# Optimization experiments

Measured on AMD Instinct MI355X. Metric: run time of the kernel, lower is better.

Reference implementation:

```python
import jax, jax.numpy as jnp
import numpy as np

E = 1024   # embd_size
H = 16     # head_count
HS = E // H
B = 8
T = 1024   # seq len == input_size
EPS = 1e-5

def _ln(x, g, b):
    m = jnp.mean(x, axis=-1, keepdims=True)
    v = jnp.mean((x - m) ** 2, axis=-1, keepdims=True)
    return (x - m) * jax.lax.rsqrt(v + EPS) * g + b

def setup_inputs() -> dict:
    key = jax.random.key(0)
    ks = jax.random.split(key, 12)
    s_attn = 1.0 / np.sqrt(E)
    s_ff1 = 1.0 / np.sqrt(E)
    s_ff2 = 1.0 / np.sqrt(4 * E)
    return {
        "x": jax.random.normal(ks[0], (B, T, E), dtype=jnp.float32),
        "wq": jax.random.normal(ks[1], (H, E, HS), dtype=jnp.float32) * s_attn,
        "wk": jax.random.normal(ks[2], (H, E, HS), dtype=jnp.float32) * s_attn,
        "wv": jax.random.normal(ks[3], (H, E, HS), dtype=jnp.float32) * s_attn,
        "w_proj": jax.random.normal(ks[4], (E, E), dtype=jnp.float32) * s_attn,
        "b_proj": jnp.zeros((E,), dtype=jnp.float32),
        "w1": jax.random.normal(ks[5], (E, 4 * E), dtype=jnp.float32) * s_ff1,
        "b1": jnp.zeros((4 * E,), dtype=jnp.float32),
        "w2": jax.random.normal(ks[6], (4 * E, E), dtype=jnp.float32) * s_ff2,
        "b2": jnp.zeros((E,), dtype=jnp.float32),
        "g1": jnp.ones((E,), dtype=jnp.float32),
        "be1": jnp.zeros((E,), dtype=jnp.float32),
        "g2": jnp.ones((E,), dtype=jnp.float32),
        "be2": jnp.zeros((E,), dtype=jnp.float32),
    }

def reference(x, wq, wk, wv, w_proj, b_proj, w1, b1, w2, b2, g1, be1, g2, be2):
    Tn = x.shape[1]
    h = _ln(x, g1, be1)
    # per-head projections, batched over heads: [B,T,E] x [H,E,S] -> [B,H,T,S]
    q = jnp.einsum('bte,hes->bhts', h, wq)
    k = jnp.einsum('bte,hes->bhts', h, wk)
    v = jnp.einsum('bte,hes->bhts', h, wv)
    scores = jnp.einsum('bhts,bhus->bhtu', q, k)
    # NOTE: source multiplies by sqrt(T) (x.shape[2] of scores), not 1/sqrt(head_size)
    scores = scores * jnp.float32(Tn) ** 0.5
    causal = jnp.tril(jnp.ones((Tn, Tn), dtype=bool))
    scores = jnp.where(causal, scores, -jnp.inf)
    attn = jax.nn.softmax(scores, axis=-1)
    out = jnp.einsum('bhtu,bhus->bhts', attn, v)           # [B,H,T,S]
    out = out.transpose(0, 2, 1, 3).reshape(x.shape[0], Tn, E)  # concat heads
    out = out @ w_proj + b_proj
    x = x + out
    f = _ln(x, g2, be2)
    f = jax.nn.relu(f @ w1 + b1) @ w2 + b2
    return x + f
```

## Files before the change

### kernel.cpp

```cpp
#include <hip/hip_runtime.h>


typedef unsigned short u16;
typedef __attribute__((ext_vector_type(8))) short  bfx8;
typedef __attribute__((ext_vector_type(4))) float  f32x4;
typedef __attribute__((ext_vector_type(4))) unsigned short u16v4;

#define MFMA16 __builtin_amdgcn_mfma_f32_16x16x32_bf16

__device__ __forceinline__ u16 f2bf(float f) {
    union { float f; unsigned u; } c; c.f = f;
    unsigned r = c.u + 0x7fffu + ((c.u >> 16) & 1u);
    return (u16)(r >> 16);
}
__device__ __forceinline__ float bf2f(u16 b) {
    union { unsigned u; float f; } c; c.u = ((unsigned)b) << 16; return c.f;
}
__device__ __forceinline__ float exp2_fast(float x) {
    float r; asm("v_exp_f32 %0, %1" : "=v"(r) : "v"(x)); return r;
}

__device__ __forceinline__ void gl_lds16(const void* g, void* l) {
    void* gg = (void*)g;
    __builtin_amdgcn_global_load_lds(
        (__attribute__((address_space(1))) void*)gg,
        (__attribute__((address_space(3))) void*)l,
        16, 0, 0);
}

__device__ __forceinline__ void transpose_tile(const float* __restrict__ src,
                                               u16* __restrict__ dhi,
                                               u16* __restrict__ dlo,
                                               int C, int OS, int row0, int col0)
{
    __shared__ float t[64][65];
    const int tid = threadIdx.x;
    const float* s = src + ((size_t)row0) * C + col0;
    const size_t obase = ((size_t)col0) * OS + row0;
    {
        const int r = tid >> 2, c4 = (tid & 3) * 16;
#pragma unroll
        for (int k = 0; k < 4; ++k) {
            float4 f = *(const float4*)(s + (size_t)r * C + c4 + k * 4);
            t[r][c4 + k*4 + 0] = f.x; t[r][c4 + k*4 + 1] = f.y;
            t[r][c4 + k*4 + 2] = f.z; t[r][c4 + k*4 + 3] = f.w;
        }
    }
    __syncthreads();
    {
        const int c = tid >> 2, r4 = (tid & 3) * 16;
        bfx8 h0, h1, l0, l1;
#pragma unroll
        for (int k = 0; k < 8; ++k) {
            float v0 = t[r4 + k][c];
            float v1 = t[r4 + 8 + k][c];
            u16 a = f2bf(v0), b = f2bf(v1);
            h0[k] = (short)a; h1[k] = (short)b;
            l0[k] = (short)f2bf(v0 - bf2f(a));
            l1[k] = (short)f2bf(v1 - bf2f(b));
        }
        u16* d = dhi + obase + (size_t)c * OS + r4;
        *(bfx8*)d = h0; *(bfx8*)(d + 8) = h1;
        if (dlo) {
            u16* d2 = dlo + obase + (size_t)c * OS + r4;
            *(bfx8*)d2 = l0; *(bfx8*)(d2 + 8) = l1;
        }
    }
}

__global__ __launch_bounds__(256)
void repack_qkv(const float* __restrict__ wq, const float* __restrict__ wk,
                const float* __restrict__ wv, u16* __restrict__ qkhi,
                u16* __restrict__ qklo, u16* __restrict__ vT)
{
    const int sel = blockIdx.x;
    const int yt  = blockIdx.y;
    const int hh  = blockIdx.z;
    const float* src = (sel == 0) ? wq : (sel == 1) ? wk : wv;
    u16* dhi = (sel == 0) ? qkhi : (sel == 1) ? (qkhi + (size_t)1024 * 1024) : vT;
    u16* dlo = (sel == 0) ? qklo : (sel == 1) ? (qklo + (size_t)1024 * 1024) : nullptr;
    transpose_tile(src + (size_t)hh * 65536,
                   dhi + (size_t)hh * 65536,
                   dlo ? dlo + (size_t)hh * 65536 : nullptr,
                   64, 1024, yt * 64, 0);
}

__global__ __launch_bounds__(256)
void repack_w(const float* __restrict__ wp, u16* __restrict__ wpT,
              const float* __restrict__ w1, u16* __restrict__ w1T,
              const float* __restrict__ w2, u16* __restrict__ w2T)
{
    const int id = blockIdx.x;
    if (id < 256) {
        const int xt = id & 15, yt = id >> 4;
        transpose_tile(wp, wpT, nullptr, 1024, 1024, yt * 64, xt * 64);
    } else if (id < 1280) {
        const int i2 = id - 256;
        const int xt = i2 & 63, yt = i2 >> 6;
        transpose_tile(w1, w1T, nullptr, 4096, 1024, yt * 64, xt * 64);
    } else {
        const int i2 = id - 1280;
        const int xt = i2 & 15, yt = i2 >> 4;
        transpose_tile(w2, w2T, nullptr, 1024, 4096, yt * 64, xt * 64);
    }
}

__global__ __launch_bounds__(256)
void ln_split(const float* __restrict__ x, const float* __restrict__ g,
              const float* __restrict__ be, u16* __restrict__ hhi,
              u16* __restrict__ hlo)
{
    const int row = blockIdx.x;
    const int tid = threadIdx.x;
    const float4 v = ((const float4*)(x + (size_t)row * 1024))[tid];
    float s  = v.x + v.y + v.z + v.w;
    float s2 = v.x*v.x + v.y*v.y + v.z*v.z + v.w*v.w;
#pragma unroll
    for (int m = 32; m >= 1; m >>= 1) {
        s  += __shfl_xor(s,  m, 64);
        s2 += __shfl_xor(s2, m, 64);
    }
    __shared__ float rs[4], rq[4];
    if ((tid & 63) == 0) { rs[tid >> 6] = s; rq[tid >> 6] = s2; }
    __syncthreads();
    s  = rs[0] + rs[1] + rs[2] + rs[3];
    s2 = rq[0] + rq[1] + rq[2] + rq[3];
    const float mean = s * (1.0f / 1024.0f);
    const float var  = s2 * (1.0f / 1024.0f) - mean * mean;
    const float inv  = rsqrtf(var + 1e-5f);
    const int col0 = tid * 4;
    float hv[4];
    hv[0] = (v.x - mean) * inv * g[col0+0] + be[col0+0];
    hv[1] = (v.y - mean) * inv * g[col0+1] + be[col0+1];
    hv[2] = (v.z - mean) * inv * g[col0+2] + be[col0+2];
    hv[3] = (v.w - mean) * inv * g[col0+3] + be[col0+3];
    u16v4 hb, lb;
#pragma unroll
    for (int k = 0; k < 4; ++k) {
        u16 a = f2bf(hv[k]);
        hb[k] = a;
        lb[k] = f2bf(hv[k] - bf2f(a));
    }
    *(u16v4*)(hhi + (size_t)row * 1024 + col0) = hb;
    if (hlo) *(u16v4*)(hlo + (size_t)row * 1024 + col0) = lb;
}

#define BM 128
#define BN 128
#define BKT 32

template<int FLAGS>
__global__ __launch_bounds__(256, 2)
void gemm_bt(const u16* __restrict__ A, const u16* __restrict__ Bt,
             void* __restrict__ Cout, const float* __restrict__ bias,
             const float* __restrict__ res, int M, int N, int K)
{
    __shared__ u16 As[BM * BKT];
    __shared__ u16 Bs[BN * BKT];
    const int tid  = threadIdx.x;
    const int lane = tid & 63, wave = tid >> 6;
    const int wr = wave >> 1, wc = wave & 1;
    const int li = lane & 15, lg = lane >> 4;

    const int nbx = gridDim.x;
    const int nwg = nbx * gridDim.y;
    const int cpx = nwg >> 3;
    int bid = blockIdx.y * nbx + blockIdx.x;
    bid = (bid & 7) * cpx + (bid >> 3);
    const size_t m0 = (size_t)(bid / nbx) * BM;
    const size_t n0 = (size_t)(bid % nbx) * BN;
    f32x4 acc[4][4] = {};

    const int slot0 = tid, slot1 = tid + 256;
    const int r0 = slot0 >> 2, kc0 = (slot0 & 3) * 8;
    const int r1 = slot1 >> 2, kc1 = (slot1 & 3) * 8;

    for (int kt = 0; kt < K; kt += BKT) {
        __syncthreads();
        gl_lds16(A  + (m0 + r0) * K + kt + kc0, As + slot0 * 8);
        gl_lds16(Bt + (n0 + r0) * K + kt + kc0, Bs + slot0 * 8);
        gl_lds16(A  + (m0 + r1) * K + kt + kc1, As + slot1 * 8);
        gl_lds16(Bt + (n0 + r1) * K + kt + kc1, Bs + slot1 * 8);
        __syncthreads();
        bfx8 af[4], bfr[4];
#pragma unroll
        for (int i = 0; i < 4; ++i)
            af[i] = *(const bfx8*)&As[(wr * 64 + i * 16 + li) * BKT + lg * 8];
#pragma unroll
        for (int j = 0; j < 4; ++j)
            bfr[j] = *(const bfx8*)&Bs[(wc * 64 + j * 16 + li) * BKT + lg * 8];
#pragma unroll
        for (int i = 0; i < 4; ++i)
#pragma unroll
            for (int j = 0; j < 4; ++j)
                acc[i][j] = MFMA16(af[i], bfr[j], acc[i][j], 0, 0, 0);
    }

    float* Cf = (float*)Cout;
    u16*   Cb = (u16*)Cout;
#pragma unroll
    for (int i = 0; i < 4; ++i)
#pragma unroll
        for (int j = 0; j < 4; ++j)
#pragma unroll
            for (int r = 0; r < 4; ++r) {
                const size_t row = m0 + wr * 64 + i * 16 + lg * 4 + r;
                const size_t col = n0 + wc * 64 + j * 16 + li;
                float v = acc[i][j][r];
                if (FLAGS & 1) v += bias[col];
                if (FLAGS & 2) v = fmaxf(v, 0.0f);
                if (FLAGS & 4) v += res[row * (size_t)N + col];
                if (FLAGS & 16) {
                    const size_t drow = ((col >> 10) * 16 + (row >> 6)) * 64 + (row & 63);
                    Cb[drow * 1024 + (col & 1023)] = f2bf(v);
                } else if (FLAGS & 8) {
                    Cf[row * (size_t)N + col] = v;
                } else {
                    Cb[row * (size_t)N + col] = f2bf(v);
                }
            }
}

template<int EPI, int SPLIT3>
__global__ __launch_bounds__(512, 2)
void gemm8(const u16* __restrict__ A, const u16* __restrict__ Al,
           const u16* __restrict__ Bt, const u16* __restrict__ Bl,
           u16* __restrict__ C, u16* __restrict__ Clo,
           const float* __restrict__ bias,
           int M, int N, int K, int NBX)
{
    __shared__ u16 Asl[2][2][128 * 64];
    __shared__ u16 Bsl[2][2][128 * 64];
    const int tid = threadIdx.x;
    const int lane = tid & 63, wave = tid >> 6;
    const int wr = wave >> 2, wc = wave & 3;
    const int li = lane & 15, lg = lane >> 4;

    const int bid = blockIdx.x;
    const int nwg = gridDim.x;
    const int cpx = nwg >> 3;
    const int swz = (bid & 7) * cpx + (bid >> 3);
    const int bx = swz % NBX, by = swz / NBX;
    const size_t m0 = (size_t)by * 256, n0 = (size_t)bx * 256;

    char* ldsA = (char*)&Asl[0][0][0];
    char* ldsB = (char*)&Bsl[0][0][0];

    const int KT = K >> 6;

    auto stageA = [&](int j, int h) {
        const u16* src = A;
        int jj = j;
        if (SPLIT3) {
            src = (j < 2 * KT) ? A : Al;
            jj = (j < KT) ? j : ((j < 2 * KT) ? j - KT : j - 2 * KT);
        }
#pragma unroll
        for (int site = 0; site < 2; ++site) {
            const int s = tid + site * 512;
            const int r = s >> 3;
            const int cb = ((s & 7) << 4) ^ ((r & 7) << 4);
            gl_lds16((const char*)(src + (m0 + h * 128 + r) * (size_t)K + (size_t)jj * 64) + cb,
                     ldsA + ((j & 1) * 2 + h) * 16384 + s * 16);
        }
    };
    auto stageB = [&](int j, int h) {
        const u16* src = Bt;
        int jj = j;
        if (SPLIT3) {
            src = (j < KT) ? Bt : ((j < 2 * KT) ? Bl : Bt);
            jj = (j < KT) ? j : ((j < 2 * KT) ? j - KT : j - 2 * KT);
        }
#pragma unroll
        for (int site = 0; site < 2; ++site) {
            const int s = tid + site * 512;
            const int r = s >> 3;
            const int cb = ((s & 7) << 4) ^ ((r & 7) << 4);
            gl_lds16((const char*)(src + (n0 + h * 128 + r) * (size_t)K + (size_t)jj * 64) + cb,
                     ldsB + ((j & 1) * 2 + h) * 16384 + s * 16);
        }
    };

    const int lsw = (li & 7) << 4;
    const int aHalfBase = wr * 16384;
    const int bHalfBase = (wc >> 1) * 16384;
    const int bRow0 = (wc & 1) * 64;

    f32x4 acc[8][4] = {};
    const int NT = SPLIT3 ? 3 * KT : KT;
    const int NI = NT >> 1;

    stageA(0, 0); stageA(0, 1); stageB(0, 0); stageB(0, 1);
    stageB(1, 0); stageB(1, 1);
    asm volatile("s_waitcnt vmcnt(0)" ::: "memory");
    __builtin_amdgcn_sched_barrier(0);
    __builtin_amdgcn_s_barrier();
    __builtin_amdgcn_sched_barrier(0);

    for (int t = 0; t < NI; ++t) {
        const bool more = (t + 1 < NI);
#pragma unroll
        for (int half = 0; half < 2; ++half) {
            const int buf = half;
            const int abase = buf * 32768 + aHalfBase;
            const int bbase = buf * 32768 + bHalfBase;
            bfx8 bfr[4][2];
#pragma unroll
            for (int q = 0; q < 4; ++q) {
                if (q == 0) {
#pragma unroll
                    for (int nf = 0; nf < 4; ++nf)
#pragma unroll
                        for (int ks = 0; ks < 2; ++ks)
                            bfr[nf][ks] = *(const bfx8*)(ldsB + bbase
                                + (bRow0 + nf * 16 + li) * 128
                                + ((ks * 64 + lg * 16) ^ lsw));
                }
                bfx8 afr[2][2];
#pragma unroll
                for (int m = 0; m < 2; ++m)
#pragma unroll
                    for (int ks = 0; ks < 2; ++ks)
                        afr[m][ks] = *(const bfx8*)(ldsA + abase
                            + ((2 * q + m) * 16 + li) * 128
                            + ((ks * 64 + lg * 16) ^ lsw));

                if (half == 0) {
                    if (q == 0) stageA(2 * t + 1, 0);
                    else if (q == 1) stageA(2 * t + 1, 1);
                    else if (q == 2) { if (more) stageB(2 * t + 2, 0); }
                    else             { if (more) stageB(2 * t + 2, 1); }
                } else {
                    if (q == 0)      { if (more) stageA(2 * t + 2, 0); }
                    else if (q == 1) { if (more) stageA(2 * t + 2, 1); }
                    else if (q == 2) { if (more) stageB(2 * t + 3, 0); }
                    else             { if (more) stageB(2 * t + 3, 1); }
                }

                __builtin_amdgcn_sched_barrier(0);
                __builtin_amdgcn_s_barrier();
                asm volatile("s_waitcnt lgkmcnt(0)" ::: "memory");
                __builtin_amdgcn_sched_barrier(0);
                __builtin_amdgcn_s_setprio(1);
#pragma unroll
                for (int ks = 0; ks < 2; ++ks)
#pragma unroll
                    for (int m = 0; m < 2; ++m)
#pragma unroll
                        for (int nf = 0; nf < 4; ++nf)
                            acc[2 * q + m][nf] = MFMA16(afr[m][ks], bfr[nf][ks],
                                                        acc[2 * q + m][nf], 0, 0, 0);
                __builtin_amdgcn_s_setprio(0);
                __builtin_amdgcn_sched_barrier(0);
                if (q == 3) {
                    if (half == 0) {
                        if (more) { asm volatile("s_waitcnt vmcnt(4)" ::: "memory"); }
                        else      { asm volatile("s_waitcnt vmcnt(0)" ::: "memory"); }
                    } else if (more) {
                        asm volatile("s_waitcnt vmcnt(4)" ::: "memory");
                    }
                    __builtin_amdgcn_sched_barrier(0);
                }
                __builtin_amdgcn_s_barrier();
                __builtin_amdgcn_sched_barrier(0);
            }
        }
    }

#pragma unroll
    for (int i = 0; i < 8; ++i)
#pragma unroll
        for (int nf = 0; nf < 4; ++nf)
#pragma unroll
            for (int r = 0; r < 4; ++r) {
                const size_t row = m0 + wr * 128 + i * 16 + lg * 4 + r;
                const size_t col = n0 + wc * 64 + nf * 16 + li;
                if (EPI == 0) {
                    float v = acc[i][nf][r] + bias[col];
                    v = fmaxf(v, 0.0f);
                    C[row * (size_t)N + col] = f2bf(v);
                } else {
                    const float v = acc[i][nf][r];
                    const u16 hi = f2bf(v);
                    C[row * (size_t)N + col]   = hi;
                    Clo[row * (size_t)N + col] = f2bf(v - bf2f(hi));
                }
            }
}

#define QKS 2048

__global__ __launch_bounds__(256, 3)
void attn(const u16* __restrict__ qkhi, const u16* __restrict__ qklo,
          const u16* __restrict__ vt, u16* __restrict__ ao)
{
    const int id  = blockIdx.x;
    const int swz = (id & 7) * 256 + (id >> 3);
    const int qt  = 15 - (swz & 15);
    const int h   = (swz >> 4) & 15;
    const int b   = swz >> 8;

    const int tid = threadIdx.x;
    const int wave = tid >> 6, lane = tid & 63;
    const int li = lane & 15, lg = lane >> 4;

    __shared__ u16 KsHi[2][4096];
    __shared__ u16 KsLo[2][4096];
    __shared__ u16 Pl[64 * 64];

    const size_t qrow = (size_t)b * 1024 + qt * 64 + wave * 16 + li;
    const size_t qoff = qrow * QKS + h * 64 + lg * 8;
    const bfx8 qh0 = *(const bfx8*)(qkhi + qoff);
    const bfx8 qh1 = *(const bfx8*)(qkhi + qoff + 32);
    const bfx8 ql0 = *(const bfx8*)(qklo + qoff);
    const bfx8 ql1 = *(const bfx8*)(qklo + qoff + 32);

    bfx8 onesf;
#pragma unroll
    for (int k = 0; k < 8; ++k) onesf[k] = (short)0x3F80;

    f32x4 O[4] = {};
    f32x4 O5 = {0.f, 0.f, 0.f, 0.f};
    float mrow[4] = {-3e38f, -3e38f, -3e38f, -3e38f};

    const u16* kh_base = qkhi + ((size_t)b * 1024) * QKS + 1024 + h * 64;
    const u16* kl_base = qklo + ((size_t)b * 1024) * QKS + 1024 + h * 64;
    const u16* v_base  = vt + ((size_t)(b * 16 + h) * 64) * 1024;

    auto stageK = [&](int kt, int bufIdx) {
#pragma unroll
        for (int site = 0; site < 2; ++site) {
            const int s = tid + site * 256;
            const int r = s >> 3;
            const int cb = (((s & 7) << 4) ^ ((r & 7) << 4));
            const size_t go = ((size_t)(kt * 64 + r)) * QKS;
            gl_lds16((const char*)(kh_base + go) + cb, (char*)&KsHi[bufIdx][0] + s * 16);
            gl_lds16((const char*)(kl_base + go) + cb, (char*)&KsLo[bufIdx][0] + s * 16);
        }
    };

    const int rswz = (li & 7) << 4;
    char* pband = (char*)&Pl[0] + wave * 2048;

    stageK(0, 0);

    for (int kt = 0; kt <= qt; ++kt) {
        const int cur = kt & 1;

        bfx8 vld[2][4];
#pragma unroll
        for (int nf = 0; nf < 4; ++nf) {
            const u16* vr = v_base + ((size_t)(nf * 16 + li)) * 1024 + kt * 64 + lg * 8;
            vld[0][nf] = *(const bfx8*)vr;
            vld[1][nf] = *(const bfx8*)(vr + 32);
        }

        if (kt < qt) {
            stageK(kt + 1, cur ^ 1);
            asm volatile("s_waitcnt vmcnt(12)" ::: "memory");
        } else {
            asm volatile("s_waitcnt vmcnt(8)" ::: "memory");
        }
        __builtin_amdgcn_sched_barrier(0);
        __builtin_amdgcn_s_barrier();
        __builtin_amdgcn_sched_barrier(0);

        float sv[4][4];
        const char* khc = (const char*)&KsHi[cur][0];
        const char* klc = (const char*)&KsLo[cur][0];
#pragma unroll
        for (int nf = 0; nf < 4; ++nf) {
            const int rb = (nf * 16 + li) * 128;
            bfx8 kh0v = *(const bfx8*)(khc + rb + (((lg * 16) + 0 ) ^ rswz));
            bfx8 kh1v = *(const bfx8*)(khc + rb + (((lg * 16) + 64) ^ rswz));
            bfx8 kl0v = *(const bfx8*)(klc + rb + (((lg * 16) + 0 ) ^ rswz));
            bfx8 kl1v = *(const bfx8*)(klc + rb + (((lg * 16) + 64) ^ rswz));
            f32x4 a = {0.f, 0.f, 0.f, 0.f};
            a = MFMA16(qh0, kh0v, a, 0, 0, 0);
            a = MFMA16(qh1, kh1v, a, 0, 0, 0);
            a = MFMA16(qh0, kl0v, a, 0, 0, 0);
            a = MFMA16(qh1, kl1v, a, 0, 0, 0);
            a = MFMA16(ql0, kh0v, a, 0, 0, 0);
            a = MFMA16(ql1, kh1v, a, 0, 0, 0);
#pragma unroll
            for (int r = 0; r < 4; ++r) sv[nf][r] = a[r];
        }

        asm volatile("s_waitcnt lgkmcnt(0)" ::: "memory");
        __builtin_amdgcn_sched_barrier(0);
        __builtin_amdgcn_s_barrier();
        __builtin_amdgcn_sched_barrier(0);

        const float SC = 46.16624130844683f;
        float pmax[4] = {-3e38f, -3e38f, -3e38f, -3e38f};
        if (kt == qt) {
            const int rowg = qt * 64 + wave * 16 + lg * 4;
            const int colg = kt * 64 + li;
#pragma unroll
            for (int nf = 0; nf < 4; ++nf)
#pragma unroll
                for (int r = 0; r < 4; ++r) {
                    float x2 = sv[nf][r] * SC;
                    if (colg + nf * 16 > rowg + r) x2 = -3e38f;
                    sv[nf][r] = x2;
                    pmax[r] = fmaxf(pmax[r], x2);
                }
        } else {
#pragma unroll
            for (int nf = 0; nf < 4; ++nf)
#pragma unroll
                for (int r = 0; r < 4; ++r) {
                    const float x2 = sv[nf][r] * SC;
                    sv[nf][r] = x2;
                    pmax[r] = fmaxf(pmax[r], x2);
                }
        }
#pragma unroll
        for (int msk = 1; msk < 16; msk <<= 1)
#pragma unroll
            for (int r = 0; r < 4; ++r)
                pmax[r] = fmaxf(pmax[r], __shfl_xor(pmax[r], msk, 64));

        const bool grow = !__all((pmax[0] - mrow[0] <= 11.5416f) &&
                                 (pmax[1] - mrow[1] <= 11.5416f) &&
                                 (pmax[2] - mrow[2] <= 11.5416f) &&
                                 (pmax[3] - mrow[3] <= 11.5416f));
        if (grow) {
            float alr[4];
#pragma unroll
            for (int r = 0; r < 4; ++r) {
                const float mnew = fmaxf(mrow[r], pmax[r]);
                alr[r] = exp2_fast(mrow[r] - mnew);
                mrow[r] = mnew;
            }
#pragma unroll
            for (int nf = 0; nf < 4; ++nf)
#pragma unroll
                for (int r = 0; r < 4; ++r)
                    O[nf][r] *= alr[r];
#pragma unroll
            for (int r = 0; r < 4; ++r)
                O5[r] *= alr[r];
        }

#pragma unroll
        for (int nf = 0; nf < 4; ++nf)
#pragma unroll
            for (int r = 0; r < 4; ++r) {
                const int prow = lg * 4 + r;
                const int pb = prow * 128 + ((((nf * 16 + li) * 2)) ^ ((prow & 7) << 4));
                *(u16*)(pband + pb) = f2bf(exp2_fast(sv[nf][r] - mrow[r]));
            }

#pragma unroll
        for (int ku = 0; ku < 2; ++ku) {
            bfx8 pf = *(const bfx8*)(pband + li * 128
                                     + ((ku * 64 + lg * 16) ^ ((li & 7) << 4)));
#pragma unroll
            for (int nf = 0; nf < 4; ++nf)
                O[nf] = MFMA16(pf, vld[ku][nf], O[nf], 0, 0, 0);
            O5 = MFMA16(pf, onesf, O5, 0, 0, 0);
        }
    }

    float invl[4];
#pragma unroll
    for (int r = 0; r < 4; ++r) invl[r] = 1.0f / O5[r];
    const size_t orow = (size_t)b * 1024 + qt * 64 + wave * 16 + lg * 4;
#pragma unroll
    for (int nf = 0; nf < 4; ++nf)
#pragma unroll
        for (int r = 0; r < 4; ++r)
            ao[(orow + r) * 1024 + h * 64 + nf * 16 + li] = f2bf(O[nf][r] * invl[r]);
}

extern "C" void kernel_launch(void* const* d_in, const int* in_sizes, int n_in,
                              void* d_out, int out_size, void* d_ws, size_t ws_size,
                              hipStream_t stream)
{
    (void)in_sizes; (void)n_in; (void)out_size; (void)ws_size;
    const float* x      = (const float*)d_in[0];
    const float* wq     = (const float*)d_in[1];
    const float* wk     = (const float*)d_in[2];
    const float* wv     = (const float*)d_in[3];
    const float* w_proj = (const float*)d_in[4];
    const float* b_proj = (const float*)d_in[5];
    const float* w1     = (const float*)d_in[6];
    const float* b1     = (const float*)d_in[7];
    const float* w2     = (const float*)d_in[8];
    const float* b2     = (const float*)d_in[9];
    const float* g1     = (const float*)d_in[10];
    const float* be1    = (const float*)d_in[11];
    const float* g2     = (const float*)d_in[12];
    const float* be2    = (const float*)d_in[13];
    float* out = (float*)d_out;

    const size_t MB = (size_t)1024 * 1024;
    char* wsp = (char*)d_ws;
    u16* h_hi  = (u16*)(wsp + 0 * MB);
    u16* h_lo  = (u16*)(wsp + 16 * MB);
    u16* qk_hi = (u16*)(wsp + 32 * MB);
    u16* qk_lo = (u16*)(wsp + 64 * MB);
    u16* vtr   = (u16*)(wsp + 112 * MB);
    float* y   = (float*)(wsp + 128 * MB);
    u16* wqkT_hi = (u16*)(wsp + 160 * MB);
    u16* wqkT_lo = (u16*)(wsp + 164 * MB);
    u16* wvT     = (u16*)(wsp + 168 * MB);
    u16* wpT     = (u16*)(wsp + 170 * MB);
    u16* w1T     = (u16*)(wsp + 172 * MB);
    u16* w2T     = (u16*)(wsp + 180 * MB);
    u16* f2  = h_hi;
    u16* ao  = h_lo;
    u16* act = qk_hi;

    dim3 blk(256);

    repack_qkv<<<dim3(3, 16, 16), blk, 0, stream>>>(wq, wk, wv, wqkT_hi, wqkT_lo, wvT);
    repack_w<<<dim3(2304), blk, 0, stream>>>(w_proj, wpT, w1, w1T, w2, w2T);

    ln_split<<<8192, blk, 0, stream>>>(x, g1, be1, h_hi, h_lo);

    gemm8<1, 1><<<dim3(256), dim3(512), 0, stream>>>(h_hi, h_lo, wqkT_hi, wqkT_lo,
                                                     qk_hi, qk_lo, nullptr,
                                                     8192, 2048, 1024, 8);
    gemm_bt<16><<<dim3(64, 8), blk, 0, stream>>>(wvT, h_hi, vtr, nullptr, nullptr, 1024, 8192, 1024);

    attn<<<dim3(2048), blk, 0, stream>>>(qk_hi, qk_lo, vtr, ao);

    gemm_bt<1 | 4 | 8><<<dim3(8, 64), blk, 0, stream>>>(ao, wpT, y, b_proj, x, 8192, 1024, 1024);

    ln_split<<<8192, blk, 0, stream>>>(y, g2, be2, f2, nullptr);

    gemm8<0, 0><<<dim3(512), dim3(512), 0, stream>>>(f2, nullptr, w1T, nullptr,
                                                     act, nullptr, b1,
                                                     8192, 4096, 1024, 16);
    gemm_bt<1 | 4 | 8><<<dim3(8, 64), blk, 0, stream>>>(act, w2T, out, b2, y, 8192, 1024, 4096);
}
```

Baseline: 489.2 us.

## Stage K in 128-row pairs and halve barriers in causal attention loop

The attention kernel now stages two 64-key tiles per iteration into double-buffered LDS (now twice as large). It overlaps the second tile's QK MFMAs with the first tile's softmax and PV work, so the loop needs half as many block barriers. The intent is to cut synchronisation and load-latency stalls per key tile. The cost is more LDS per block (about 72KB), which may lower occupancy below the 3-blocks launch bound, plus more registers held for the second V tile.

```diff
diff --git a/kernel.cpp b/kernel.cpp
--- a/kernel.cpp
+++ b/kernel.cpp
@@ -404,8 +404,8 @@
     const int wave = tid >> 6, lane = tid & 63;
     const int li = lane & 15, lg = lane >> 4;
 
-    __shared__ u16 KsHi[2][4096];
-    __shared__ u16 KsLo[2][4096];
+    __shared__ u16 KsHi[2][8192];
+    __shared__ u16 KsLo[2][8192];
     __shared__ u16 Pl[64 * 64];
 
     const size_t qrow = (size_t)b * 1024 + qt * 64 + wave * 16 + li;
@@ -427,13 +427,13 @@
     const u16* kl_base = qklo + ((size_t)b * 1024) * QKS + 1024 + h * 64;
     const u16* v_base  = vt + ((size_t)(b * 16 + h) * 64) * 1024;
 
-    auto stageK = [&](int kt, int bufIdx) {
-#pragma unroll
-        for (int site = 0; site < 2; ++site) {
+    auto stagePair = [&](int p, int bufIdx) {
+#pragma unroll
+        for (int site = 0; site < 4; ++site) {
             const int s = tid + site * 256;
             const int r = s >> 3;
             const int cb = (((s & 7) << 4) ^ ((r & 7) << 4));
-            const size_t go = ((size_t)(kt * 64 + r)) * QKS;
+            const size_t go = ((size_t)(p * 128 + r)) * QKS;
             gl_lds16((const char*)(kh_base + go) + cb, (char*)&KsHi[bufIdx][0] + s * 16);
             gl_lds16((const char*)(kl_base + go) + cb, (char*)&KsLo[bufIdx][0] + s * 16);
         }
@@ -442,22 +442,100 @@
     const int rswz = (li & 7) << 4;
     char* pband = (char*)&Pl[0] + wave * 2048;
 
-    stageK(0, 0);
-
-    for (int kt = 0; kt <= qt; ++kt) {
-        const int cur = kt & 1;
-
-        bfx8 vld[2][4];
+    const float SC = 46.16624130844683f;
+
+    auto processTile = [&](float (&sv)[4][4], int kt, bfx8 (&vldX)[2][4]) {
+        float pmax[4] = {-3e38f, -3e38f, -3e38f, -3e38f};
+        if (kt == qt) {
+            const int rowg = qt * 64 + wave * 16 + lg * 4;
+            const int colg = kt * 64 + li;
+#pragma unroll
+            for (int nf = 0; nf < 4; ++nf)
+#pragma unroll
+                for (int r = 0; r < 4; ++r) {
+                    float x2 = sv[nf][r] * SC;
+                    if (colg + nf * 16 > rowg + r) x2 = -3e38f;
+                    sv[nf][r] = x2;
+                    pmax[r] = fmaxf(pmax[r], x2);
+                }
+        } else {
+#pragma unroll
+            for (int nf = 0; nf < 4; ++nf)
+#pragma unroll
+                for (int r = 0; r < 4; ++r) {
+                    const float x2 = sv[nf][r] * SC;
+                    sv[nf][r] = x2;
+                    pmax[r] = fmaxf(pmax[r], x2);
+                }
+        }
+#pragma unroll
+        for (int msk = 1; msk < 16; msk <<= 1)
+#pragma unroll
+            for (int r = 0; r < 4; ++r)
+                pmax[r] = fmaxf(pmax[r], __shfl_xor(pmax[r], msk, 64));
+
+        const bool grow = !__all((pmax[0] - mrow[0] <= 11.5416f) &&
+                                 (pmax[1] - mrow[1] <= 11.5416f) &&
+                                 (pmax[2] - mrow[2] <= 11.5416f) &&
+                                 (pmax[3] - mrow[3] <= 11.5416f));
+        if (grow) {
+            float alr[4];
+#pragma unroll
+            for (int r = 0; r < 4; ++r) {
+                const float mnew = fmaxf(mrow[r], pmax[r]);
+                alr[r] = exp2_fast(mrow[r] - mnew);
+                mrow[r] = mnew;
+            }
+#pragma unroll
+            for (int nf = 0; nf < 4; ++nf)
+#pragma unroll
+                for (int r = 0; r < 4; ++r)
+                    O[nf][r] *= alr[r];
+#pragma unroll
+            for (int r = 0; r < 4; ++r)
+                O5[r] *= alr[r];
+        }
+
+#pragma unroll
+        for (int nf = 0; nf < 4; ++nf)
+#pragma unroll
+            for (int r = 0; r < 4; ++r) {
+                const int prow = lg * 4 + r;
+                const int pb = prow * 128 + ((((nf * 16 + li) * 2)) ^ ((prow & 7) << 4));
+                *(u16*)(pband + pb) = f2bf(exp2_fast(sv[nf][r] - mrow[r]));
+            }
+
+#pragma unroll
+        for (int ku = 0; ku < 2; ++ku) {
+            bfx8 pf = *(const bfx8*)(pband + li * 128
+                                     + ((ku * 64 + lg * 16) ^ ((li & 7) << 4)));
+#pragma unroll
+            for (int nf = 0; nf < 4; ++nf)
+                O[nf] = MFMA16(pf, vldX[ku][nf], O[nf], 0, 0, 0);
+            O5 = MFMA16(pf, onesf, O5, 0, 0, 0);
+        }
+    };
+
+    const int nkt = qt + 1;
+    const int np  = (nkt + 1) >> 1;
+    stagePair(0, 0);
+
+    for (int p = 0; p < np; ++p) {
+        const int cur = p & 1;
+        const int kt0 = 2 * p;
+        const bool has1 = (kt0 + 1 < nkt);
+
+        bfx8 vld0[2][4];
 #pragma unroll
         for (int nf = 0; nf < 4; ++nf) {
-            const u16* vr = v_base + ((size_t)(nf * 16 + li)) * 1024 + kt * 64 + lg * 8;
-            vld[0][nf] = *(const bfx8*)vr;
-            vld[1][nf] = *(const bfx8*)(vr + 32);
-        }
-
-        if (kt < qt) {
-            stageK(kt + 1, cur ^ 1);
-            asm volatile("s_waitcnt vmcnt(12)" ::: "memory");
+            const u16* vr = v_base + ((size_t)(nf * 16 + li)) * 1024 + kt0 * 64 + lg * 8;
+            vld0[0][nf] = *(const bfx8*)vr;
+            vld0[1][nf] = *(const bfx8*)(vr + 32);
+        }
+
+        if (p + 1 < np) {
+            stagePair(p + 1, cur ^ 1);
+            asm volatile("s_waitcnt vmcnt(16)" ::: "memory");
         } else {
             asm volatile("s_waitcnt vmcnt(8)" ::: "memory");
         }
@@ -465,9 +543,10 @@
         __builtin_amdgcn_s_barrier();
         __builtin_amdgcn_sched_barrier(0);
 
-        float sv[4][4];
         const char* khc = (const char*)&KsHi[cur][0];
         const char* klc = (const char*)&KsLo[cur][0];
+
+        float sv[4][4];
 #pragma unroll
         for (int nf = 0; nf < 4; ++nf) {
             const int rb = (nf * 16 + li) * 128;
@@ -486,81 +565,45 @@
             for (int r = 0; r < 4; ++r) sv[nf][r] = a[r];
         }
 
+        bfx8 vld1[2][4];
+        if (has1) {
+#pragma unroll
+            for (int nf = 0; nf < 4; ++nf) {
+                const u16* vr = v_base + ((size_t)(nf * 16 + li)) * 1024 + (kt0 + 1) * 64 + lg * 8;
+                vld1[0][nf] = *(const bfx8*)vr;
+                vld1[1][nf] = *(const bfx8*)(vr + 32);
+            }
+        }
+
+        processTile(sv, kt0, vld0);
+
+        if (has1) {
+#pragma unroll
+            for (int nf = 0; nf < 4; ++nf) {
+                const int rb = (64 + nf * 16 + li) * 128;
+                bfx8 kh0v = *(const bfx8*)(khc + rb + (((lg * 16) + 0 ) ^ rswz));
+                bfx8 kh1v = *(const bfx8*)(khc + rb + (((lg * 16) + 64) ^ rswz));
+                bfx8 kl0v = *(const bfx8*)(klc + rb + (((lg * 16) + 0 ) ^ rswz));
+                bfx8 kl1v = *(const bfx8*)(klc + rb + (((lg * 16) + 64) ^ rswz));
+                f32x4 a = {0.f, 0.f, 0.f, 0.f};
+                a = MFMA16(qh0, kh0v, a, 0, 0, 0);
+                a = MFMA16(qh1, kh1v, a, 0, 0, 0);
+                a = MFMA16(qh0, kl0v, a, 0, 0, 0);
+                a = MFMA16(qh1, kl1v, a, 0, 0, 0);
+                a = MFMA16(ql0, kh0v, a, 0, 0, 0);
+                a = MFMA16(ql1, kh1v, a, 0, 0, 0);
+#pragma unroll
+                for (int r = 0; r < 4; ++r) sv[nf][r] = a[r];
+            }
+        }
+
         asm volatile("s_waitcnt lgkmcnt(0)" ::: "memory");
         __builtin_amdgcn_sched_barrier(0);
         __builtin_amdgcn_s_barrier();
         __builtin_amdgcn_sched_barrier(0);
 
-        const float SC = 46.16624130844683f;
-        float pmax[4] = {-3e38f, -3e38f, -3e38f, -3e38f};
-        if (kt == qt) {
-            const int rowg = qt * 64 + wave * 16 + lg * 4;
-            const int colg = kt * 64 + li;
-#pragma unroll
-            for (int nf = 0; nf < 4; ++nf)
-#pragma unroll
-                for (int r = 0; r < 4; ++r) {
-                    float x2 = sv[nf][r] * SC;
-                    if (colg + nf * 16 > rowg + r) x2 = -3e38f;
-                    sv[nf][r] = x2;
-                    pmax[r] = fmaxf(pmax[r], x2);
-                }
-        } else {
-#pragma unroll
-            for (int nf = 0; nf < 4; ++nf)
-#pragma unroll
-                for (int r = 0; r < 4; ++r) {
-                    const float x2 = sv[nf][r] * SC;
-                    sv[nf][r] = x2;
-                    pmax[r] = fmaxf(pmax[r], x2);
-                }
-        }
-#pragma unroll
-        for (int msk = 1; msk < 16; msk <<= 1)
-#pragma unroll
-            for (int r = 0; r < 4; ++r)
-                pmax[r] = fmaxf(pmax[r], __shfl_xor(pmax[r], msk, 64));
-
-        const bool grow = !__all((pmax[0] - mrow[0] <= 11.5416f) &&
-                                 (pmax[1] - mrow[1] <= 11.5416f) &&
-                                 (pmax[2] - mrow[2] <= 11.5416f) &&
-                                 (pmax[3] - mrow[3] <= 11.5416f));
-        if (grow) {
-            float alr[4];
-#pragma unroll
-            for (int r = 0; r < 4; ++r) {
-                const float mnew = fmaxf(mrow[r], pmax[r]);
-                alr[r] = exp2_fast(mrow[r] - mnew);
-                mrow[r] = mnew;
-            }
-#pragma unroll
-            for (int nf = 0; nf < 4; ++nf)
-#pragma unroll
-                for (int r = 0; r < 4; ++r)
-                    O[nf][r] *= alr[r];
-#pragma unroll
-            for (int r = 0; r < 4; ++r)
-                O5[r] *= alr[r];
-        }
-
-#pragma unroll
-        for (int nf = 0; nf < 4; ++nf)
-#pragma unroll
-            for (int r = 0; r < 4; ++r) {
-                const int prow = lg * 4 + r;
-                const int pb = prow * 128 + ((((nf * 16 + li) * 2)) ^ ((prow & 7) << 4));
-                *(u16*)(pband + pb) = f2bf(exp2_fast(sv[nf][r] - mrow[r]));
-            }
-
-#pragma unroll
-        for (int ku = 0; ku < 2; ++ku) {
-            bfx8 pf = *(const bfx8*)(pband + li * 128
-                                     + ((ku * 64 + lg * 16) ^ ((li & 7) << 4)));
-#pragma unroll
-            for (int nf = 0; nf < 4; ++nf)
-                O[nf] = MFMA16(pf, vld[ku][nf], O[nf], 0, 0, 0);
-            O5 = MFMA16(pf, onesf, O5, 0, 0, 0);
-        }
+        if (has1)
+            processTile(sv, kt0 + 1, vld1);
     }
 
     float invl[4];
```

Result: no change. 495.3 us (+1.2%).
